# Performance work log

Hardware: AMD Instinct MI355X
Metric: run time of the kernel (lower is better)

The kernel has to match this reference:

```python
import jax, jax.numpy as jnp
import numpy as np

B = 30          # bandwidth
L = B           # degrees l = 0..L-1
NB = 2 * B      # spatial grid size per angle (beta/alpha/gamma)
MW = 2 * L - 1  # centered frequency index width, m in [-(L-1), L-1]
P = 6           # kernel grid points (n_alpha=6, n_beta=1)


def _wigner_d_all(betas, L):
    """Wigner-d matrices d^l_{m,n}(beta) via d^l(beta)=expm(-(beta/2)(J+ - J-)).
    Returns [len(betas), L, MW, MW], zero-padded for |m|,|n|>l."""
    betas = np.asarray(betas, dtype=np.float64)
    D = np.zeros((len(betas), L, MW, MW), dtype=np.float64)
    for l in range(L):
        dim = 2 * l + 1
        m = np.arange(-l, l)
        cp = np.sqrt(l * (l + 1) - m * (m + 1))  # <m+1|J+|m>
        A = np.zeros((dim, dim))
        A[np.arange(1, dim), np.arange(dim - 1)] = cp
        A = A - A.T  # J+ - J-, real antisymmetric
        lam, V = np.linalg.eigh(1j * A)  # Hermitian
        ph = np.exp(0.5j * betas[:, None] * lam[None, :])  # [nb, dim]
        dl = np.einsum('ab,jb,cb->jac', V, ph, V.conj()).real
        off = L - 1 - l
        D[:, l, off:off + dim, off:off + dim] = dl
    return D


def _s3_quadrature(b):
    """SOFT-grid quadrature weights over beta (lie_learn S3 formula, up to a constant)."""
    j = np.arange(2 * b)
    k = np.arange(b)[None, :]
    s = (np.sin(np.pi * (2 * j[:, None] + 1) * (2 * k + 1) / (4 * b)) / (2 * k + 1)).sum(axis=1)
    return (2.0 / b) * np.sin(np.pi * (2 * j + 1) / (4 * b)) * s


# ---- precomputed constants ----
_betas_sig = np.pi * (2 * np.arange(NB) + 1) / (4 * B)  # SOFT beta grid
_D_np = _wigner_d_all(_betas_sig, L)                    # [NB, L, MW, MW]
_alphas_k = np.linspace(0.0, 2.0 * np.pi, P, endpoint=False)
_Dk_np = _wigner_d_all(np.full(P, np.pi / 160.0), L)[:, :, :, L - 1]  # [P, L, MW], n=0 column
_idx_c = (np.arange(MW) - (L - 1)) % NB                 # centered m -> FFT bin
_nidx = np.arange(MW) - (L - 1)

D_SIG = jnp.asarray(_D_np, dtype=jnp.float32)
D0_SIG = jnp.asarray(_D_np[:, :, :, L - 1], dtype=jnp.float32)
D_KER = jnp.asarray(_Dk_np, dtype=jnp.float32)
W_QUAD = jnp.asarray(_s3_quadrature(B), dtype=jnp.float32)
FAC_L = jnp.asarray(2 * np.arange(L) + 1, dtype=jnp.float32)
E_KER = jnp.asarray(np.exp(-1j * _nidx[None, :] * _alphas_k[:, None]), dtype=jnp.complex64)


def s2_conv(x, wk):
    """FFT-based S2 convolution: S2 analysis -> spectral multiply -> SO(3) synthesis.
    x: [batch, f_in, NB(beta), NB(alpha)] real; wk: [f_in, f_out, P].
    Returns [batch, f_out, NB(beta), NB(alpha), NB(gamma)] real."""
    xf = jnp.fft.fft(x, axis=-1) * (2.0 * np.pi / NB)        # alpha -> m, complex64
    xfc = xf[..., _idx_c]                                     # centered m: [b,f,NB,MW]
    # S2 analysis: X^l_m = sum_beta w(beta) d^l_{m0}(beta) xhat(beta, m)
    X = jnp.einsum('j,jlm,bfjm->bflm', W_QUAD, D0_SIG, xfc)   # [b,f_in,L,MW]
    # kernel spectrum psi^l_n = sum_p wk_p d^l_{n0}(beta_p) e^{-i n alpha_p}
    psi = jnp.einsum('iop,pln,pn->ioln', wk.astype(jnp.complex64),
                     D_KER.astype(jnp.complex64), E_KER)      # [f_in,f_out,L,MW]
    # spectral mm: Z^l_{mn} = sum_{f_in} X^l_m conj(psi^l_n)
    Z = jnp.einsum('bilm,ioln->bolmn', X, jnp.conj(psi))      # [b,f_out,L,MW,MW]
    # SO(3) synthesis per beta: F(beta,m,n) = sum_l (2l+1) d^l_{mn}(beta) Z^l_{mn}
    F = jnp.einsum('l,jlmn,bolmn->bojmn', FAC_L, D_SIG, Z)    # [b,f_out,NB,MW,MW]
    G = jnp.zeros(F.shape[:3] + (NB, NB), dtype=F.dtype)
    G = G.at[..., _idx_c[:, None], _idx_c[None, :]].set(F)    # embed centered freqs
    return jnp.fft.ifft2(G, axes=(-2, -1)).real * float(NB * NB)


def so3_integrate_gamma(x):
    # matches the given so3_integrate: contracts ONLY the last (gamma) axis with w
    return jnp.einsum('...g,g->...', x, W_QUAD)


def setup_inputs() -> dict:
    key = jax.random.key(0)
    k1, k2, k3 = jax.random.split(key, 3)
    batch = 16
    x1 = jax.random.normal(k1, (batch, 2, NB, NB), dtype=jnp.float32)
    w_conv = jax.random.normal(k2, (2, 10, P), dtype=jnp.float32) / np.sqrt(2 * P)
    w_deconv = jax.random.normal(k3, (10, 2, P), dtype=jnp.float32) / np.sqrt(10 * P)
    return {"x1": x1, "w_conv": w_conv, "w_deconv": w_deconv}


def reference(x1, w_conv, w_deconv):
    x = s2_conv(x1, w_conv)        # encode: [b,10,60,60,60]
    x = so3_integrate_gamma(x)     # [b,10,60,60] (S2 signal)
    x = s2_conv(x, w_deconv)       # decode: [b,2,60,60,60]
    return so3_integrate_gamma(x)  # [b,2,60,60]
```

## Files before the change

kernel.cpp:

```cpp
#include <hip/hip_runtime.h>
#include <hip/hip_fp16.h>

#define NBG   60
#define LMAX  30
#define MWC   59
#define CTR   29
#define NPAIR 20
#define NT    11
#define NTP   12
#define NOFF  5
#define PI_F  3.14159265358979323846f

__device__ void wigner_colf(float beta, int mp, int mn, float scale,
                            float* out, int stride) {
  int a = mp - mn; if (a < 0) a = -a;
  int b = mp + mn; if (b < 0) b = -b;
  int lmin = (a + b) >> 1;
  for (int l = 0; l < LMAX; ++l) out[l * stride] = 0.0f;
  if (lmin >= LMAX) return;
  float sh, ch; sincosf(0.5f * beta, &sh, &ch);
  float x = ch * ch - sh * sh;
  float base = scale;
  for (int q = 0; q < a; ++q) base *= sh;
  for (int q = 0; q < b; ++q) base *= ch;
  if (mp >= mn && ((mp - mn) & 1)) base = -base;
  float K2 = 1.f;
  for (int q = 1; q <= a; ++q) K2 *= (float)(b + q) / (float)q;
  float Pm2 = 0.f, Pm1 = 1.f;
  out[lmin * stride] = base * sqrtf(K2);
  for (int s = 1; lmin + s < LMAX; ++s) {
    float Ps;
    if (s == 1) {
      Ps = (a + 1) + (a + b + 2) * 0.5f * (x - 1.f);
    } else {
      float t0 = 2.f * s + a + b;
      float c1 = 2.f * s * (s + a + b) * (t0 - 2.f);
      float c2 = (t0 - 1.f) * (t0 * (t0 - 2.f) * x + (float)(a * a - b * b));
      float c3 = 2.f * (s + a - 1.f) * (s + b - 1.f) * t0;
      Ps = (c2 * Pm1 - c3 * Pm2) / c1;
    }
    K2 *= ((float)s * (s + a + b)) / (((float)s + a) * ((float)s + b));
    out[(lmin + s) * stride] = base * sqrtf(K2) * Ps;
    Pm2 = Pm1; Pm1 = Ps;
  }
}

__device__ __forceinline__ float quad_w(int j) {
  float s = 0.f;
  for (int k = 0; k < 30; ++k) {
    int r = ((2 * j + 1) * (2 * k + 1)) % 240;
    s += sinf(2.f * PI_F * r / 240.f) / (float)(2 * k + 1);
  }
  return (2.f / 30.f) * sinf(PI_F * (2 * j + 1) / 120.f) * s;
}

__global__ __launch_bounds__(256)
void k1_prep(const float* __restrict__ x1,
             const float* __restrict__ wc, const float* __restrict__ wd,
             float2* __restrict__ scwF1, float2* __restrict__ scwF2,
             float* __restrict__ D0T, float* __restrict__ sgd,
             float2* __restrict__ xfT) {
  __shared__ __align__(16) char smem[23104];
  int bi = blockIdx.x, t = threadIdx.x;

  if (bi == 0) {
    float*  swq  = (float*)smem;
    float2* swqn = (float2*)(smem + 240);
    if (t < NBG) swq[t] = quad_w(t);
    __syncthreads();
    if (t < NT) {
      int n = t - NOFF;
      float re = 0.f, im = 0.f;
      for (int g = 0; g < NBG; ++g) {
        int k = ((n * g) % NBG + NBG) % NBG;
        float sn, cs; sincosf(2.f * PI_F * k / 60.f, &sn, &cs);
        re += swq[g] * cs; im += swq[g] * sn;
      }
      swqn[t] = make_float2(re, im);
    }
    __syncthreads();
    if (t < NT * NPAIR) {
      int nn = t / NPAIR, pair = t - nn * NPAIR, n = nn - NOFF;
      float re1 = 0, im1 = 0, re2 = 0, im2 = 0;
      for (int p = 0; p < 6; ++p) {
        int k = ((n * p) % 6 + 6) % 6;
        float sn, cs; sincosf(2.f * PI_F * k / 6.f, &sn, &cs);
        float a1 = wc[pair * 6 + p], a2 = wd[pair * 6 + p];
        re1 += a1 * cs; im1 += a1 * sn;
        re2 += a2 * cs; im2 += a2 * sn;
      }
      float2 w = swqn[nn];
      scwF1[t] = make_float2(w.x * re1 - w.y * im1, w.x * im1 + w.y * re1);
      scwF2[t] = make_float2(PI_F * (w.x * re2 - w.y * im2),
                             PI_F * (w.x * im2 + w.y * re2));
    }
  } else if (bi < 60) {
    int M = bi - 1;
    if (t < NBG) {
      float wqj = quad_w(t);
      wigner_colf(PI_F * (2 * t + 1) / 120.f, M - CTR, 0, wqj,
                  D0T + (size_t)M * LMAX * NBG + t, NBG);
    }
  } else if (bi < 180) {
    float* buf  = (float*)smem;
    float* dkwL = (float*)(smem + 21600);
    int s = bi - 60, j = s >> 1, Mq = s & 1;
    if (t < 15 * NT) {
      int Mi = t / NT, nn = t - Mi * NT;
      int mp = Mq * 15 + Mi - CTR, mn = nn - NOFF;
      wigner_colf(PI_F * (2 * j + 1) / 120.f, mp, mn, 1.f,
                  &buf[Mi * LMAX * NTP + nn], NTP);
    } else if (t >= 165 && t < 165 + NT) {
      int nn = t - 165;
      wigner_colf(PI_F / 160.f, nn - NOFF, 0, 1.f, dkwL + nn, NTP);
      for (int l = 0; l < LMAX; ++l) dkwL[l * NTP + nn] *= (float)(2 * l + 1);
    }
    __syncthreads();
    size_t base = (size_t)(j * 30 + Mq * 15) * LMAX * NTP;
    for (int q = t; q < 15 * LMAX * NTP; q += 256) {
      int r = q % (LMAX * NTP), l = r / NTP, nn = r - l * NTP;
      float v = (nn < NT) ? buf[q] * dkwL[l * NTP + nn] : 0.f;
      sgd[base + q] = v;
    }
  } else {
    float*  xr  = (float*)smem;
    float*  twc = (float*)(smem + 1920);
    float*  tws = (float*)(smem + 2160);
    float2* xo  = (float2*)(smem + 2400);
    int s = bi - 180, j = s >> 2, qh = s & 3;
    for (int q = t; q < 8 * NBG; q += 256) {
      int bl = q / NBG, a = q - bl * NBG;
      xr[bl * NBG + a] = x1[((size_t)(qh * 8 + bl) * NBG + j) * NBG + a];
    }
    if (t < NBG) {
      float sn, cs; sincosf(-2.f * PI_F * t / 60.f, &sn, &cs);
      twc[t] = cs; tws[t] = sn;
    }
    __syncthreads();
    for (int q = t; q < 8 * MWC; q += 256) {
      int bl = q / MWC, M = q - bl * MWC, mm = M - CTR;
      const float* xp = xr + bl * NBG;
      float re = 0.f, im = 0.f; int k = 0;
      for (int a = 0; a < NBG; ++a) {
        re += xp[a] * twc[k]; im += xp[a] * tws[k];
        k += mm; if (k >= NBG) k -= NBG; if (k < 0) k += NBG;
      }
      const float sc = 2.f * PI_F / 60.f;
      xo[M * 9 + bl] = make_float2(re * sc, im * sc);
    }
    __syncthreads();
    for (int q = t; q < MWC * 8; q += 256) {
      int M = q / 8, bl = q - M * 8;
      xfT[((size_t)M * NBG + j) * 32 + qh * 8 + bl] = xo[M * 9 + bl];
    }
  }
}

__global__ __launch_bounds__(256)
void k_ana1(const float2* __restrict__ xfT, const float* __restrict__ D0T,
            float2* __restrict__ X21) {
  __shared__ float2 sxf[NBG][32];
  __shared__ float  sD[8][NBG];
  int M = blockIdx.x >> 2, lq = blockIdx.x & 3;
  int t = threadIdx.x;
  for (int q = t; q < NBG * 32; q += 256) ((float2*)sxf)[q] = xfT[(size_t)M * NBG * 32 + q];
  for (int q = t; q < 8 * NBG; q += 256) {
    int ll = q / NBG, jj = q - ll * NBG, l = lq * 8 + ll;
    sD[ll][jj] = (l < LMAX) ? D0T[((size_t)M * LMAX + l) * NBG + jj] : 0.f;
  }
  __syncthreads();
  int ll = t >> 5, w = t & 31, i = w >> 4, b = w & 15;
  int l = lq * 8 + ll;
  if (l < LMAX) {
    float re = 0.f, im = 0.f;
#pragma unroll 6
    for (int jj = 0; jj < NBG; ++jj) {
      float d = sD[ll][jj];
      float2 v = sxf[jj][b * 2 + i];
      re += d * v.x; im += d * v.y;
    }
    X21[(size_t)M * LMAX * 32 + l * 32 + w] = make_float2(re, im);
  }
}

__global__ __launch_bounds__(256)
void k_core1(const float2* __restrict__ X2, const float* __restrict__ sgd,
             const float2* __restrict__ scwF, __half2* __restrict__ Th) {
  __shared__ float  sg[2][LMAX][NTP];
  __shared__ float2 scw[NT * NPAIR];
  __shared__ float2 sC[2][LMAX][NPAIR];
  __shared__ float2 sX[2][LMAX][32];
  int t = threadIdx.x;
  int j = blockIdx.x / 30, mg = blockIdx.x - 30 * j;
  int Mbase = mg * 2;

  for (int q = t; q < NT * NPAIR; q += 256) scw[q] = scwF[q];
  for (int q = t; q < 2 * LMAX * 32; q += 256) {
    int Mi = q / (LMAX * 32), r = q - Mi * (LMAX * 32);
    int M = Mbase + Mi;
    ((float2*)sX)[q] = (M < MWC) ? X2[(size_t)M * LMAX * 32 + r]
                                 : make_float2(0.f, 0.f);
  }
  for (int q = t; q < 2 * LMAX * NTP; q += 256) {
    int Mi = q / (LMAX * NTP), r = q - Mi * LMAX * NTP;
    int l = r / NTP, nn = r - l * NTP;
    int M = Mbase + Mi;
    float v = 0.f;
    if (M < MWC && nn < NT) {
      if (M < 30) {
        v = sgd[(size_t)(j * 30 + M) * LMAX * NTP + r];
      } else {
        v = sgd[(size_t)(j * 30 + 58 - M) * LMAX * NTP + l * NTP + (10 - nn)];
        if (!(M & 1)) v = -v;
      }
    }
    ((float*)sg)[q] = v;
  }
  __syncthreads();

  for (int q = t; q < 2 * LMAX * NPAIR; q += 256) {
    int Mi = q / (LMAX * NPAIR), r = q - Mi * LMAX * NPAIR;
    int l = r / NPAIR, pair = r - l * NPAIR;
    float cre = 0.f, cim = 0.f;
#pragma unroll
    for (int nn = 0; nn < NT; ++nn) {
      float g = sg[Mi][l][nn];
      float2 c = scw[nn * NPAIR + pair];
      cre += g * c.x; cim += g * c.y;
    }
    ((float2*)sC)[q] = make_float2(cre, cim);
  }
  __syncthreads();

  for (int q = t; q < 2 * 160; q += 256) {
    int Mi = q / 160, u = q - Mi * 160;
    int M = Mbase + Mi;
    if (M >= MWC) continue;
    int bb = u / 10, o = u - 10 * bb;
    float tre = 0.f, tim = 0.f;
#pragma unroll 6
    for (int l = 0; l < LMAX; ++l) {
#pragma unroll
      for (int i = 0; i < 2; ++i) {
        float2 xv = sX[Mi][l][i * 16 + bb];
        float2 cv = sC[Mi][l][i * 10 + o];
        tre += xv.x * cv.x - xv.y * cv.y;
        tim += xv.x * cv.y + xv.y * cv.x;
      }
    }
    Th[((size_t)j * MWC + M) * 160 + u] = __floats2half2_rn(tre, tim);
  }
}

__global__ __launch_bounds__(256)
void k_ana2(const __half2* __restrict__ T1, const float* __restrict__ D0T,
            float2* __restrict__ X22) {
  __shared__ float2 sxf[NBG][40];
  __shared__ float  sD[LMAX][NBG];
  int M = blockIdx.x >> 2, q4 = blockIdx.x & 3;
  int u0 = q4 * 40, t = threadIdx.x;
  for (int q = t; q < NBG * 40; q += 256) {
    int jj = q / 40, uq = q - jj * 40;
    float2 v1 = __half22float2(T1[((size_t)jj * MWC + M) * 160 + u0 + uq]);
    float2 v2 = __half22float2(T1[((size_t)jj * MWC + (58 - M)) * 160 + u0 + uq]);
    sxf[jj][uq] = make_float2(v1.x + v2.x, v1.y - v2.y);
  }
  for (int q = t; q < LMAX * NBG; q += 256) ((float*)sD)[q] = D0T[(size_t)M * LMAX * NBG + q];
  __syncthreads();
  for (int q = t; q < LMAX * 40; q += 256) {
    int l = q / 40, w = q - l * 40;
    float re = 0.f, im = 0.f;
#pragma unroll 6
    for (int jj = 0; jj < NBG; ++jj) {
      float d = sD[l][jj];
      float2 v = sxf[jj][w];
      re += d * v.x; im += d * v.y;
    }
    int uu = u0 + w;
    int p = (uu % 10) * 16 + uu / 10;
    X22[((size_t)M * LMAX + l) * 160 + p] = make_float2(re, im);
  }
}

__global__ __launch_bounds__(256)
void k_core2(const float2* __restrict__ X2, const float* __restrict__ sgd,
             const float2* __restrict__ scwF, float2* __restrict__ Tf) {
  __shared__ float  sg[2][LMAX][NTP];
  __shared__ float2 scw[NT * NPAIR];
  __shared__ float2 sC[2][LMAX][NPAIR];
  __shared__ float2 sRed[256];
  int t = threadIdx.x;
  int j = blockIdx.x / 30, mg = blockIdx.x - 30 * j;
  int Mbase = mg * 2;

  for (int q = t; q < NT * NPAIR; q += 256) scw[q] = scwF[q];
  for (int q = t; q < 2 * LMAX * NTP; q += 256) {
    int Mi = q / (LMAX * NTP), r = q - Mi * LMAX * NTP;
    int l = r / NTP, nn = r - l * NTP;
    int M = Mbase + Mi;
    float v = 0.f;
    if (M < MWC && nn < NT) {
      if (M < 30) {
        v = sgd[(size_t)(j * 30 + M) * LMAX * NTP + r];
      } else {
        v = sgd[(size_t)(j * 30 + 58 - M) * LMAX * NTP + l * NTP + (10 - nn)];
        if (!(M & 1)) v = -v;
      }
    }
    ((float*)sg)[q] = v;
  }
  __syncthreads();

  for (int q = t; q < 2 * LMAX * NPAIR; q += 256) {
    int Mi = q / (LMAX * NPAIR), r = q - Mi * LMAX * NPAIR;
    int l = r / NPAIR, pair = r - l * NPAIR;
    float cre = 0.f, cim = 0.f;
#pragma unroll
    for (int nn = 0; nn < NT; ++nn) {
      float g = sg[Mi][l][nn];
      float2 c = scw[nn * NPAIR + pair];
      cre += g * c.x; cim += g * c.y;
    }
    ((float2*)sC)[q] = make_float2(cre, cim);
  }
  __syncthreads();

  int sub = t >> 6, idx = t & 63;
  int Mi = idx >> 5, u = idx & 31;
  int M = Mbase + Mi;
  int bb = u >> 1, o = u & 1;
  float tre = 0.f, tim = 0.f;
  if (M < MWC) {
    for (int l = sub; l < LMAX; l += 4) {
#pragma unroll
      for (int i = 0; i < 10; ++i) {
        float2 xv = X2[((size_t)M * LMAX + l) * 160 + i * 16 + bb];
        float2 cv = sC[Mi][l][i * 2 + o];
        tre += xv.x * cv.x - xv.y * cv.y;
        tim += xv.x * cv.y + xv.y * cv.x;
      }
    }
  }
  sRed[t] = make_float2(tre, tim);
  __syncthreads();
  if (t < 64 && M < MWC) {
    float2 a0 = sRed[t], a1 = sRed[t + 64], a2 = sRed[t + 128], a3 = sRed[t + 192];
    Tf[((size_t)j * MWC + M) * 32 + u] =
        make_float2(a0.x + a1.x + a2.x + a3.x, a0.y + a1.y + a2.y + a3.y);
  }
}

__global__ __launch_bounds__(256)
void k_synth2(const float2* __restrict__ T2, float* __restrict__ out) {
  __shared__ float2 sT[MWC][16];
  __shared__ float twc[NBG], tws[NBG];
  int j = blockIdx.x >> 1, uh = blockIdx.x & 1;
  int u0 = uh * 16, t = threadIdx.x;
  for (int q = t; q < MWC * 16; q += 256) {
    int M = q / 16, uu = q - M * 16;
    sT[M][uu] = T2[((size_t)j * MWC + M) * 32 + u0 + uu];
  }
  if (t < NBG) {
    float s, c; sincosf(2.f * PI_F * t / 60.f, &s, &c);
    twc[t] = c; tws[t] = s;
  }
  __syncthreads();
  for (int q = t; q < 16 * NBG; q += 256) {
    int uu = q / NBG, a = q - uu * NBG;
    int k = (31 * a) % NBG;
    float acc = 0.f;
#pragma unroll 4
    for (int M = 0; M < MWC; ++M) {
      float2 v = sT[M][uu];
      acc += v.x * twc[k] - v.y * tws[k];
      k += a; if (k >= NBG) k -= NBG;
    }
    out[((size_t)(u0 + uu) * NBG + j) * NBG + a] = acc;
  }
}

extern "C" void kernel_launch(void* const* d_in, const int* in_sizes, int n_in,
                              void* d_out, int out_size, void* d_ws, size_t ws_size,
                              hipStream_t stream) {
  const float* x1       = (const float*)d_in[0];
  const float* w_conv   = (const float*)d_in[1];
  const float* w_deconv = (const float*)d_in[2];
  float* out = (float*)d_out;
  char* ws = (char*)d_ws;

  float2*  scwF1 = (float2*) (ws + 0);
  float2*  scwF2 = (float2*) (ws + 2048);
  float*   D0T   = (float*)  (ws + 4096);
  float*   sgd   = (float*)  (ws + 430080);
  char*    R1    = ws + 3022592;
  char*    R2    = ws + 5288192;
  float2*  X21   = (float2*) (ws + 7553792);
  float2*  xfT   = (float2*) R1;
  float2*  X22   = (float2*) R1;
  __half2* T1    = (__half2*)R2;
  float2*  T2    = (float2*) R2;

  k1_prep<<<420, 256, 0, stream>>>(x1, w_conv, w_deconv, scwF1, scwF2, D0T, sgd, xfT);
  k_ana1<<<236, 256, 0, stream>>>(xfT, D0T, X21);
  k_core1<<<1800, 256, 0, stream>>>(X21, sgd, scwF1, T1);
  k_ana2<<<236, 256, 0, stream>>>(T1, D0T, X22);
  k_core2<<<1800, 256, 0, stream>>>(X22, sgd, scwF2, T2);
  k_synth2<<<120, 256, 0, stream>>>(T2, out);
}
```

Baseline: 101.0 us.

## Fuse six kernels into one cooperative persistent kernel with grid syncs

Merges the six stage kernels into a single cooperative persistent kernel that loops over work units per phase and separates phases with grid-wide barriers. It also re-splits the sgd-prep and ana2 work into more, smaller units and moves core1's X reads from shared memory to direct global loads. The goal is to remove the per-launch overhead and inter-kernel gaps. In exchange, the grid is capped by occupancy, so the 1800-unit phases run in fewer waves, grid syncs have their own cost, and a fallback multi-launch path is kept.

```diff
diff --git a/kernel.cpp b/kernel.cpp
--- a/kernel.cpp
+++ b/kernel.cpp
@@ -1,5 +1,8 @@
 #include <hip/hip_runtime.h>
 #include <hip/hip_fp16.h>
+#include <hip/hip_cooperative_groups.h>
+
+namespace cg = cooperative_groups;
 
 #define NBG   60
 #define LMAX  30
@@ -10,6 +13,7 @@
 #define NTP   12
 #define NOFF  5
 #define PI_F  3.14159265358979323846f
+#define SMEM_BYTES 17408
 
 __device__ void wigner_colf(float beta, int mp, int mn, float scale,
                             float* out, int stride) {
@@ -54,119 +58,113 @@
   return (2.f / 30.f) * sinf(PI_F * (2 * j + 1) / 120.f) * s;
 }
 
-__global__ __launch_bounds__(256)
-void k1_prep(const float* __restrict__ x1,
-             const float* __restrict__ wc, const float* __restrict__ wd,
-             float2* __restrict__ scwF1, float2* __restrict__ scwF2,
-             float* __restrict__ D0T, float* __restrict__ sgd,
-             float2* __restrict__ xfT) {
-  __shared__ __align__(16) char smem[23104];
-  int bi = blockIdx.x, t = threadIdx.x;
-
-  if (bi == 0) {
-    float*  swq  = (float*)smem;
-    float2* swqn = (float2*)(smem + 240);
-    if (t < NBG) swq[t] = quad_w(t);
-    __syncthreads();
-    if (t < NT) {
-      int n = t - NOFF;
-      float re = 0.f, im = 0.f;
-      for (int g = 0; g < NBG; ++g) {
-        int k = ((n * g) % NBG + NBG) % NBG;
-        float sn, cs; sincosf(2.f * PI_F * k / 60.f, &sn, &cs);
-        re += swq[g] * cs; im += swq[g] * sn;
-      }
-      swqn[t] = make_float2(re, im);
-    }
-    __syncthreads();
-    if (t < NT * NPAIR) {
-      int nn = t / NPAIR, pair = t - nn * NPAIR, n = nn - NOFF;
-      float re1 = 0, im1 = 0, re2 = 0, im2 = 0;
-      for (int p = 0; p < 6; ++p) {
-        int k = ((n * p) % 6 + 6) % 6;
-        float sn, cs; sincosf(2.f * PI_F * k / 6.f, &sn, &cs);
-        float a1 = wc[pair * 6 + p], a2 = wd[pair * 6 + p];
-        re1 += a1 * cs; im1 += a1 * sn;
-        re2 += a2 * cs; im2 += a2 * sn;
-      }
-      float2 w = swqn[nn];
-      scwF1[t] = make_float2(w.x * re1 - w.y * im1, w.x * im1 + w.y * re1);
-      scwF2[t] = make_float2(PI_F * (w.x * re2 - w.y * im2),
-                             PI_F * (w.x * im2 + w.y * re2));
-    }
-  } else if (bi < 60) {
-    int M = bi - 1;
-    if (t < NBG) {
-      float wqj = quad_w(t);
-      wigner_colf(PI_F * (2 * t + 1) / 120.f, M - CTR, 0, wqj,
-                  D0T + (size_t)M * LMAX * NBG + t, NBG);
-    }
-  } else if (bi < 180) {
-    float* buf  = (float*)smem;
-    float* dkwL = (float*)(smem + 21600);
-    int s = bi - 60, j = s >> 1, Mq = s & 1;
-    if (t < 15 * NT) {
-      int Mi = t / NT, nn = t - Mi * NT;
-      int mp = Mq * 15 + Mi - CTR, mn = nn - NOFF;
-      wigner_colf(PI_F * (2 * j + 1) / 120.f, mp, mn, 1.f,
-                  &buf[Mi * LMAX * NTP + nn], NTP);
-    } else if (t >= 165 && t < 165 + NT) {
-      int nn = t - 165;
-      wigner_colf(PI_F / 160.f, nn - NOFF, 0, 1.f, dkwL + nn, NTP);
-      for (int l = 0; l < LMAX; ++l) dkwL[l * NTP + nn] *= (float)(2 * l + 1);
-    }
-    __syncthreads();
-    size_t base = (size_t)(j * 30 + Mq * 15) * LMAX * NTP;
-    for (int q = t; q < 15 * LMAX * NTP; q += 256) {
-      int r = q % (LMAX * NTP), l = r / NTP, nn = r - l * NTP;
-      float v = (nn < NT) ? buf[q] * dkwL[l * NTP + nn] : 0.f;
-      sgd[base + q] = v;
-    }
-  } else {
-    float*  xr  = (float*)smem;
-    float*  twc = (float*)(smem + 1920);
-    float*  tws = (float*)(smem + 2160);
-    float2* xo  = (float2*)(smem + 2400);
-    int s = bi - 180, j = s >> 2, qh = s & 3;
-    for (int q = t; q < 8 * NBG; q += 256) {
-      int bl = q / NBG, a = q - bl * NBG;
-      xr[bl * NBG + a] = x1[((size_t)(qh * 8 + bl) * NBG + j) * NBG + a];
-    }
-    if (t < NBG) {
-      float sn, cs; sincosf(-2.f * PI_F * t / 60.f, &sn, &cs);
-      twc[t] = cs; tws[t] = sn;
-    }
-    __syncthreads();
-    for (int q = t; q < 8 * MWC; q += 256) {
-      int bl = q / MWC, M = q - bl * MWC, mm = M - CTR;
-      const float* xp = xr + bl * NBG;
-      float re = 0.f, im = 0.f; int k = 0;
-      for (int a = 0; a < NBG; ++a) {
-        re += xp[a] * twc[k]; im += xp[a] * tws[k];
-        k += mm; if (k >= NBG) k -= NBG; if (k < 0) k += NBG;
-      }
-      const float sc = 2.f * PI_F / 60.f;
-      xo[M * 9 + bl] = make_float2(re * sc, im * sc);
-    }
-    __syncthreads();
-    for (int q = t; q < MWC * 8; q += 256) {
-      int M = q / 8, bl = q - M * 8;
-      xfT[((size_t)M * NBG + j) * 32 + qh * 8 + bl] = xo[M * 9 + bl];
-    }
-  }
-}
-
-__global__ __launch_bounds__(256)
-void k_ana1(const float2* __restrict__ xfT, const float* __restrict__ D0T,
-            float2* __restrict__ X21) {
-  __shared__ float2 sxf[NBG][32];
-  __shared__ float  sD[8][NBG];
-  int M = blockIdx.x >> 2, lq = blockIdx.x & 3;
-  int t = threadIdx.x;
-  for (int q = t; q < NBG * 32; q += 256) ((float2*)sxf)[q] = xfT[(size_t)M * NBG * 32 + q];
+
+__device__ void ph_tables(const float* wc, const float* wd,
+                          float2* scwF1, float2* scwF2, char* smem, int t) {
+  float*  swq  = (float*)smem;
+  float2* swqn = (float2*)(smem + 256);
+  if (t < NBG) swq[t] = quad_w(t);
+  __syncthreads();
+  if (t < NT) {
+    int n = t - NOFF;
+    float re = 0.f, im = 0.f;
+    for (int g = 0; g < NBG; ++g) {
+      int k = ((n * g) % NBG + NBG) % NBG;
+      float sn, cs; sincosf(2.f * PI_F * k / 60.f, &sn, &cs);
+      re += swq[g] * cs; im += swq[g] * sn;
+    }
+    swqn[t] = make_float2(re, im);
+  }
+  __syncthreads();
+  if (t < NT * NPAIR) {
+    int nn = t / NPAIR, pair = t - nn * NPAIR, n = nn - NOFF;
+    float re1 = 0, im1 = 0, re2 = 0, im2 = 0;
+    for (int p = 0; p < 6; ++p) {
+      int k = ((n * p) % 6 + 6) % 6;
+      float sn, cs; sincosf(2.f * PI_F * k / 6.f, &sn, &cs);
+      float a1 = wc[pair * 6 + p], a2 = wd[pair * 6 + p];
+      re1 += a1 * cs; im1 += a1 * sn;
+      re2 += a2 * cs; im2 += a2 * sn;
+    }
+    float2 w = swqn[nn];
+    scwF1[t] = make_float2(w.x * re1 - w.y * im1, w.x * im1 + w.y * re1);
+    scwF2[t] = make_float2(PI_F * (w.x * re2 - w.y * im2),
+                           PI_F * (w.x * im2 + w.y * re2));
+  }
+}
+
+__device__ void ph_d0t(int M, float* D0T, int t) {
+  if (t < NBG) {
+    float wqj = quad_w(t);
+    wigner_colf(PI_F * (2 * t + 1) / 120.f, M - CTR, 0, wqj,
+                D0T + (size_t)M * LMAX * NBG + t, NBG);
+  }
+}
+
+__device__ void ph_sgd(int s, float* sgd, char* smem, int t) {
+  float* buf  = (float*)smem;
+  float* dkwL = (float*)(smem + 11520);
+  int j = s >> 2, c = s & 3;
+  int M0 = c * 8, nM = (c < 3) ? 8 : 6;
+  if (t < nM * NT) {
+    int Mi = t / NT, nn = t - Mi * NT;
+    wigner_colf(PI_F * (2 * j + 1) / 120.f, M0 + Mi - CTR, nn - NOFF, 1.f,
+                &buf[Mi * 360 + nn], NTP);
+  } else if (t >= 128 && t < 128 + NT) {
+    int nn = t - 128;
+    wigner_colf(PI_F / 160.f, nn - NOFF, 0, 1.f, dkwL + nn, NTP);
+    for (int l = 0; l < LMAX; ++l) dkwL[l * NTP + nn] *= (float)(2 * l + 1);
+  }
+  __syncthreads();
+  size_t base = (size_t)(j * 30 + M0) * 360;
+  for (int q = t; q < nM * 360; q += 256) {
+    int r = q % 360, nn = r % NTP;
+    sgd[base + q] = (nn < NT) ? buf[q] * dkwL[r] : 0.f;
+  }
+}
+
+__device__ void ph_dft(int s, const float* x1, float2* xfT, char* smem, int t) {
+  float*  xr  = (float*)smem;
+  float*  twc = (float*)(smem + 1920);
+  float*  tws = (float*)(smem + 2160);
+  float2* xo  = (float2*)(smem + 2400);
+  int j = s >> 2, qh = s & 3;
+  for (int q = t; q < 8 * NBG; q += 256) {
+    int bl = q / NBG, a = q - bl * NBG;
+    xr[bl * NBG + a] = x1[((size_t)(qh * 8 + bl) * NBG + j) * NBG + a];
+  }
+  if (t < NBG) {
+    float sn, cs; sincosf(-2.f * PI_F * t / 60.f, &sn, &cs);
+    twc[t] = cs; tws[t] = sn;
+  }
+  __syncthreads();
+  for (int q = t; q < 8 * MWC; q += 256) {
+    int bl = q / MWC, M = q - bl * MWC, mm = M - CTR;
+    const float* xp = xr + bl * NBG;
+    float re = 0.f, im = 0.f; int k = 0;
+    for (int a = 0; a < NBG; ++a) {
+      re += xp[a] * twc[k]; im += xp[a] * tws[k];
+      k += mm; if (k >= NBG) k -= NBG; if (k < 0) k += NBG;
+    }
+    const float sc = 2.f * PI_F / 60.f;
+    xo[M * 9 + bl] = make_float2(re * sc, im * sc);
+  }
+  __syncthreads();
+  for (int q = t; q < MWC * 8; q += 256) {
+    int M = q / 8, bl = q - M * 8;
+    xfT[((size_t)M * NBG + j) * 32 + qh * 8 + bl] = xo[M * 9 + bl];
+  }
+}
+
+__device__ void ph_ana1(int unit, const float2* xfT, const float* D0T,
+                        float2* X21, char* smem, int t) {
+  float2* sxf = (float2*)smem;
+  float*  sD  = (float*)(smem + 15360);
+  int M = unit >> 2, lq = unit & 3;
+  for (int q = t; q < NBG * 32; q += 256) sxf[q] = xfT[(size_t)M * NBG * 32 + q];
   for (int q = t; q < 8 * NBG; q += 256) {
     int ll = q / NBG, jj = q - ll * NBG, l = lq * 8 + ll;
-    sD[ll][jj] = (l < LMAX) ? D0T[((size_t)M * LMAX + l) * NBG + jj] : 0.f;
+    sD[q] = (l < LMAX) ? D0T[((size_t)M * LMAX + l) * NBG + jj] : 0.f;
   }
   __syncthreads();
   int ll = t >> 5, w = t & 31, i = w >> 4, b = w & 15;
@@ -175,63 +173,57 @@
     float re = 0.f, im = 0.f;
 #pragma unroll 6
     for (int jj = 0; jj < NBG; ++jj) {
-      float d = sD[ll][jj];
-      float2 v = sxf[jj][b * 2 + i];
+      float d = sD[ll * NBG + jj];
+      float2 v = sxf[jj * 32 + b * 2 + i];
       re += d * v.x; im += d * v.y;
     }
     X21[(size_t)M * LMAX * 32 + l * 32 + w] = make_float2(re, im);
   }
 }
 
-__global__ __launch_bounds__(256)
-void k_core1(const float2* __restrict__ X2, const float* __restrict__ sgd,
-             const float2* __restrict__ scwF, __half2* __restrict__ Th) {
-  __shared__ float  sg[2][LMAX][NTP];
-  __shared__ float2 scw[NT * NPAIR];
-  __shared__ float2 sC[2][LMAX][NPAIR];
-  __shared__ float2 sX[2][LMAX][32];
-  int t = threadIdx.x;
-  int j = blockIdx.x / 30, mg = blockIdx.x - 30 * j;
-  int Mbase = mg * 2;
-
+__device__ void core_common(int j, int Mbase, const float* sgd,
+                            const float2* scwF, float* sg, float2* scw,
+                            float2* sC, int t) {
   for (int q = t; q < NT * NPAIR; q += 256) scw[q] = scwF[q];
-  for (int q = t; q < 2 * LMAX * 32; q += 256) {
-    int Mi = q / (LMAX * 32), r = q - Mi * (LMAX * 32);
-    int M = Mbase + Mi;
-    ((float2*)sX)[q] = (M < MWC) ? X2[(size_t)M * LMAX * 32 + r]
-                                 : make_float2(0.f, 0.f);
-  }
-  for (int q = t; q < 2 * LMAX * NTP; q += 256) {
-    int Mi = q / (LMAX * NTP), r = q - Mi * LMAX * NTP;
+  for (int q = t; q < 2 * 360; q += 256) {
+    int Mi = q / 360, r = q - Mi * 360;
     int l = r / NTP, nn = r - l * NTP;
     int M = Mbase + Mi;
     float v = 0.f;
     if (M < MWC && nn < NT) {
       if (M < 30) {
-        v = sgd[(size_t)(j * 30 + M) * LMAX * NTP + r];
+        v = sgd[(size_t)(j * 30 + M) * 360 + r];
       } else {
-        v = sgd[(size_t)(j * 30 + 58 - M) * LMAX * NTP + l * NTP + (10 - nn)];
+        v = sgd[(size_t)(j * 30 + 58 - M) * 360 + l * NTP + (10 - nn)];
         if (!(M & 1)) v = -v;
       }
     }
-    ((float*)sg)[q] = v;
-  }
-  __syncthreads();
-
+    sg[q] = v;
+  }
+  __syncthreads();
   for (int q = t; q < 2 * LMAX * NPAIR; q += 256) {
     int Mi = q / (LMAX * NPAIR), r = q - Mi * LMAX * NPAIR;
     int l = r / NPAIR, pair = r - l * NPAIR;
     float cre = 0.f, cim = 0.f;
 #pragma unroll
     for (int nn = 0; nn < NT; ++nn) {
-      float g = sg[Mi][l][nn];
+      float g = sg[Mi * 360 + l * NTP + nn];
       float2 c = scw[nn * NPAIR + pair];
       cre += g * c.x; cim += g * c.y;
     }
-    ((float2*)sC)[q] = make_float2(cre, cim);
-  }
-  __syncthreads();
-
+    sC[q] = make_float2(cre, cim);
+  }
+  __syncthreads();
+}
+
+__device__ void ph_core1(int unit, const float2* X2, const float* sgd,
+                         const float2* scwF, __half2* Th, char* smem, int t) {
+  float*  sg  = (float*)smem;
+  float2* scw = (float2*)(smem + 2880);
+  float2* sC  = (float2*)(smem + 4640);
+  int j = unit / 30, mg = unit - 30 * j;
+  int Mbase = mg * 2;
+  core_common(j, Mbase, sgd, scwF, sg, scw, sC, t);
   for (int q = t; q < 2 * 160; q += 256) {
     int Mi = q / 160, u = q - Mi * 160;
     int M = Mbase + Mi;
@@ -242,8 +234,8 @@
     for (int l = 0; l < LMAX; ++l) {
 #pragma unroll
       for (int i = 0; i < 2; ++i) {
-        float2 xv = sX[Mi][l][i * 16 + bb];
-        float2 cv = sC[Mi][l][i * 10 + o];
+        float2 xv = X2[((size_t)M * LMAX + l) * 32 + i * 16 + bb];
+        float2 cv = sC[(Mi * LMAX + l) * NPAIR + i * 10 + o];
         tre += xv.x * cv.x - xv.y * cv.y;
         tim += xv.x * cv.y + xv.y * cv.x;
       }
@@ -252,28 +244,27 @@
   }
 }
 
-__global__ __launch_bounds__(256)
-void k_ana2(const __half2* __restrict__ T1, const float* __restrict__ D0T,
-            float2* __restrict__ X22) {
-  __shared__ float2 sxf[NBG][40];
-  __shared__ float  sD[LMAX][NBG];
-  int M = blockIdx.x >> 2, q4 = blockIdx.x & 3;
-  int u0 = q4 * 40, t = threadIdx.x;
-  for (int q = t; q < NBG * 40; q += 256) {
-    int jj = q / 40, uq = q - jj * 40;
+__device__ void ph_ana2(int unit, const __half2* T1, const float* D0T,
+                        float2* X22, char* smem, int t) {
+  float2* sxf = (float2*)smem;
+  float*  sD  = (float*)(smem + 9600);
+  int M = unit >> 3, c = unit & 7;
+  int u0 = c * 20;
+  for (int q = t; q < NBG * 20; q += 256) {
+    int jj = q / 20, uq = q - jj * 20;
     float2 v1 = __half22float2(T1[((size_t)jj * MWC + M) * 160 + u0 + uq]);
     float2 v2 = __half22float2(T1[((size_t)jj * MWC + (58 - M)) * 160 + u0 + uq]);
-    sxf[jj][uq] = make_float2(v1.x + v2.x, v1.y - v2.y);
-  }
-  for (int q = t; q < LMAX * NBG; q += 256) ((float*)sD)[q] = D0T[(size_t)M * LMAX * NBG + q];
-  __syncthreads();
-  for (int q = t; q < LMAX * 40; q += 256) {
-    int l = q / 40, w = q - l * 40;
+    sxf[q] = make_float2(v1.x + v2.x, v1.y - v2.y);
+  }
+  for (int q = t; q < LMAX * NBG; q += 256) sD[q] = D0T[(size_t)M * LMAX * NBG + q];
+  __syncthreads();
+  for (int q = t; q < LMAX * 20; q += 256) {
+    int l = q / 20, w = q - l * 20;
     float re = 0.f, im = 0.f;
 #pragma unroll 6
     for (int jj = 0; jj < NBG; ++jj) {
-      float d = sD[l][jj];
-      float2 v = sxf[jj][w];
+      float d = sD[l * NBG + jj];
+      float2 v = sxf[jj * 20 + w];
       re += d * v.x; im += d * v.y;
     }
     int uu = u0 + w;
@@ -282,49 +273,15 @@
   }
 }
 
-__global__ __launch_bounds__(256)
-void k_core2(const float2* __restrict__ X2, const float* __restrict__ sgd,
-             const float2* __restrict__ scwF, float2* __restrict__ Tf) {
-  __shared__ float  sg[2][LMAX][NTP];
-  __shared__ float2 scw[NT * NPAIR];
-  __shared__ float2 sC[2][LMAX][NPAIR];
-  __shared__ float2 sRed[256];
-  int t = threadIdx.x;
-  int j = blockIdx.x / 30, mg = blockIdx.x - 30 * j;
+__device__ void ph_core2(int unit, const float2* X2, const float* sgd,
+                         const float2* scwF, float2* Tf, char* smem, int t) {
+  float*  sg   = (float*)smem;
+  float2* scw  = (float2*)(smem + 2880);
+  float2* sC   = (float2*)(smem + 4640);
+  float2* sRed = (float2*)(smem + 14240);
+  int j = unit / 30, mg = unit - 30 * j;
   int Mbase = mg * 2;
-
-  for (int q = t; q < NT * NPAIR; q += 256) scw[q] = scwF[q];
-  for (int q = t; q < 2 * LMAX * NTP; q += 256) {
-    int Mi = q / (LMAX * NTP), r = q - Mi * LMAX * NTP;
-    int l = r / NTP, nn = r - l * NTP;
-    int M = Mbase + Mi;
-    float v = 0.f;
-    if (M < MWC && nn < NT) {
-      if (M < 30) {
-        v = sgd[(size_t)(j * 30 + M) * LMAX * NTP + r];
-      } else {
-        v = sgd[(size_t)(j * 30 + 58 - M) * LMAX * NTP + l * NTP + (10 - nn)];
-        if (!(M & 1)) v = -v;
-      }
-    }
-    ((float*)sg)[q] = v;
-  }
-  __syncthreads();
-
-  for (int q = t; q < 2 * LMAX * NPAIR; q += 256) {
-    int Mi = q / (LMAX * NPAIR), r = q - Mi * LMAX * NPAIR;
-    int l = r / NPAIR, pair = r - l * NPAIR;
-    float cre = 0.f, cim = 0.f;
-#pragma unroll
-    for (int nn = 0; nn < NT; ++nn) {
-      float g = sg[Mi][l][nn];
-      float2 c = scw[nn * NPAIR + pair];
-      cre += g * c.x; cim += g * c.y;
-    }
-    ((float2*)sC)[q] = make_float2(cre, cim);
-  }
-  __syncthreads();
-
+  core_common(j, Mbase, sgd, scwF, sg, scw, sC, t);
   int sub = t >> 6, idx = t & 63;
   int Mi = idx >> 5, u = idx & 31;
   int M = Mbase + Mi;
@@ -335,7 +292,7 @@
 #pragma unroll
       for (int i = 0; i < 10; ++i) {
         float2 xv = X2[((size_t)M * LMAX + l) * 160 + i * 16 + bb];
-        float2 cv = sC[Mi][l][i * 2 + o];
+        float2 cv = sC[(Mi * LMAX + l) * NPAIR + i * 2 + o];
         tre += xv.x * cv.x - xv.y * cv.y;
         tim += xv.x * cv.y + xv.y * cv.x;
       }
@@ -350,15 +307,15 @@
   }
 }
 
-__global__ __launch_bounds__(256)
-void k_synth2(const float2* __restrict__ T2, float* __restrict__ out) {
-  __shared__ float2 sT[MWC][16];
-  __shared__ float twc[NBG], tws[NBG];
-  int j = blockIdx.x >> 1, uh = blockIdx.x & 1;
-  int u0 = uh * 16, t = threadIdx.x;
+__device__ void ph_synth(int unit, const float2* T2, float* out, char* smem, int t) {
+  float2* sT  = (float2*)smem;
+  float*  twc = (float*)(smem + 7552);
+  float*  tws = (float*)(smem + 7792);
+  int j = unit >> 1, uh = unit & 1;
+  int u0 = uh * 16;
   for (int q = t; q < MWC * 16; q += 256) {
     int M = q / 16, uu = q - M * 16;
-    sT[M][uu] = T2[((size_t)j * MWC + M) * 32 + u0 + uu];
+    sT[q] = T2[((size_t)j * MWC + M) * 32 + u0 + uu];
   }
   if (t < NBG) {
     float s, c; sincosf(2.f * PI_F * t / 60.f, &s, &c);
@@ -371,20 +328,85 @@
     float acc = 0.f;
 #pragma unroll 4
     for (int M = 0; M < MWC; ++M) {
-      float2 v = sT[M][uu];
+      float2 v = sT[M * 16 + uu];
       acc += v.x * twc[k] - v.y * tws[k];
       k += a; if (k >= NBG) k -= NBG;
     }
     out[((size_t)(u0 + uu) * NBG + j) * NBG + a] = acc;
   }
+}
+
+__device__ __forceinline__ void phaseA_dispatch(int u, const float* x1,
+    const float* wc, const float* wd, float2* scwF1, float2* scwF2,
+    float* D0T, float* sgd, float2* xfT, char* smem, int t) {
+  if (u == 0)       ph_tables(wc, wd, scwF1, scwF2, smem, t);
+  else if (u < 60)  ph_d0t(u - 1, D0T, t);
+  else if (u < 300) ph_sgd(u - 60, sgd, smem, t);
+  else              ph_dft(u - 300, x1, xfT, smem, t);
+}
+
+__global__ __launch_bounds__(256)
+void k_all(const float* x1, const float* wc, const float* wd,
+           float2* scwF1, float2* scwF2, float* D0T, float* sgd,
+           float2* xfT, float2* X21, __half2* T1, float2* X22,
+           float2* T2, float* out) {
+  __shared__ __align__(16) char smem[SMEM_BYTES];
+  cg::grid_group g = cg::this_grid();
+  int t = threadIdx.x, G = gridDim.x;
+  for (int u = blockIdx.x; u < 540; u += G) {
+    phaseA_dispatch(u, x1, wc, wd, scwF1, scwF2, D0T, sgd, xfT, smem, t);
+    __syncthreads();
+  }
+  g.sync();
+  for (int u = blockIdx.x; u < 236; u += G) { ph_ana1(u, xfT, D0T, X21, smem, t); __syncthreads(); }
+  g.sync();
+  for (int u = blockIdx.x; u < 1800; u += G) { ph_core1(u, X21, sgd, scwF1, T1, smem, t); __syncthreads(); }
+  g.sync();
+  for (int u = blockIdx.x; u < 472; u += G) { ph_ana2(u, T1, D0T, X22, smem, t); __syncthreads(); }
+  g.sync();
+  for (int u = blockIdx.x; u < 1800; u += G) { ph_core2(u, X22, sgd, scwF2, T2, smem, t); __syncthreads(); }
+  g.sync();
+  for (int u = blockIdx.x; u < 120; u += G) { ph_synth(u, T2, out, smem, t); __syncthreads(); }
+}
+
+__global__ __launch_bounds__(256)
+void kf_A(const float* x1, const float* wc, const float* wd, float2* scwF1,
+          float2* scwF2, float* D0T, float* sgd, float2* xfT) {
+  __shared__ __align__(16) char smem[SMEM_BYTES];
+  phaseA_dispatch(blockIdx.x, x1, wc, wd, scwF1, scwF2, D0T, sgd, xfT, smem, threadIdx.x);
+}
+__global__ __launch_bounds__(256)
+void kf_ana1(const float2* xfT, const float* D0T, float2* X21) {
+  __shared__ __align__(16) char smem[SMEM_BYTES];
+  ph_ana1(blockIdx.x, xfT, D0T, X21, smem, threadIdx.x);
+}
+__global__ __launch_bounds__(256)
+void kf_core1(const float2* X2, const float* sgd, const float2* scwF, __half2* Th) {
+  __shared__ __align__(16) char smem[SMEM_BYTES];
+  ph_core1(blockIdx.x, X2, sgd, scwF, Th, smem, threadIdx.x);
+}
+__global__ __launch_bounds__(256)
+void kf_ana2(const __half2* T1, const float* D0T, float2* X22) {
+  __shared__ __align__(16) char smem[SMEM_BYTES];
+  ph_ana2(blockIdx.x, T1, D0T, X22, smem, threadIdx.x);
+}
+__global__ __launch_bounds__(256)
+void kf_core2(const float2* X2, const float* sgd, const float2* scwF, float2* Tf) {
+  __shared__ __align__(16) char smem[SMEM_BYTES];
+  ph_core2(blockIdx.x, X2, sgd, scwF, Tf, smem, threadIdx.x);
+}
+__global__ __launch_bounds__(256)
+void kf_synth(const float2* T2, float* out) {
+  __shared__ __align__(16) char smem[SMEM_BYTES];
+  ph_synth(blockIdx.x, T2, out, smem, threadIdx.x);
 }
 
 extern "C" void kernel_launch(void* const* d_in, const int* in_sizes, int n_in,
                               void* d_out, int out_size, void* d_ws, size_t ws_size,
                               hipStream_t stream) {
-  const float* x1       = (const float*)d_in[0];
-  const float* w_conv   = (const float*)d_in[1];
-  const float* w_deconv = (const float*)d_in[2];
+  const float* x1 = (const float*)d_in[0];
+  const float* wc = (const float*)d_in[1];
+  const float* wd = (const float*)d_in[2];
   float* out = (float*)d_out;
   char* ws = (char*)d_ws;
 
@@ -400,10 +422,36 @@
   __half2* T1    = (__half2*)R2;
   float2*  T2    = (float2*) R2;
 
-  k1_prep<<<420, 256, 0, stream>>>(x1, w_conv, w_deconv, scwF1, scwF2, D0T, sgd, xfT);
-  k_ana1<<<236, 256, 0, stream>>>(xfT, D0T, X21);
-  k_core1<<<1800, 256, 0, stream>>>(X21, sgd, scwF1, T1);
-  k_ana2<<<236, 256, 0, stream>>>(T1, D0T, X22);
-  k_core2<<<1800, 256, 0, stream>>>(X22, sgd, scwF2, T2);
-  k_synth2<<<120, 256, 0, stream>>>(T2, out);
-}
+  int maxB = 0;
+  hipError_t qerr = hipOccupancyMaxActiveBlocksPerMultiprocessor(
+      &maxB, (const void*)k_all, 256, 0);
+  int nCU = 0;
+  int dev = 0;
+  (void)hipGetDevice(&dev);
+  if (hipDeviceGetAttribute(&nCU, hipDeviceAttributeMultiprocessorCount, dev)
+          != hipSuccess || nCU <= 0)
+    nCU = 256;
+
+  bool coop_ok = false;
+  if (qerr == hipSuccess && maxB > 0) {
+    int G = maxB * nCU;
+    if (G > 1800) G = 1800;
+    void* params[] = {
+        (void*)&x1, (void*)&wc, (void*)&wd, (void*)&scwF1, (void*)&scwF2,
+        (void*)&D0T, (void*)&sgd, (void*)&xfT, (void*)&X21, (void*)&T1,
+        (void*)&X22, (void*)&T2, (void*)&out};
+    hipError_t lerr = hipLaunchCooperativeKernel(
+        (const void*)k_all, dim3(G), dim3(256), params, 0, stream);
+    if (lerr == hipSuccess) coop_ok = true;
+    else (void)hipGetLastError();
+  }
+
+  if (!coop_ok) {
+    kf_A    <<<540,  256, 0, stream>>>(x1, wc, wd, scwF1, scwF2, D0T, sgd, xfT);
+    kf_ana1 <<<236,  256, 0, stream>>>(xfT, D0T, X21);
+    kf_core1<<<1800, 256, 0, stream>>>(X21, sgd, scwF1, T1);
+    kf_ana2 <<<472,  256, 0, stream>>>(T1, D0T, X22);
+    kf_core2<<<1800, 256, 0, stream>>>(X22, sgd, scwF2, T2);
+    kf_synth<<<120,  256, 0, stream>>>(T2, out);
+  }
+}
```

New measurement: 395.3 us. 3.92x slower.
